# Performance work log

Measured on AMD Instinct MI355X. Metric: run time of the kernel, lower is better.

The kernel has to match this reference:

```python
import jax, jax.numpy as jnp
import numpy as np


def setup_inputs() -> dict:
    key = jax.random.key(0)
    ks = jax.random.split(key, 12)
    B, H, C, D, G, F = 2, 32, 256, 128, 2048, 128
    inp = {
        'k_c': jax.random.normal(ks[0], (B, H, C, D), jnp.float32),
        'v_c': jax.random.normal(ks[1], (B, H, C, D), jnp.float32),
        'fk_c': jax.random.uniform(ks[2], (B, H, C, F), jnp.float32),
        'score_c': jax.random.uniform(ks[3], (B, H, C), jnp.float32),
        'K_win': jax.random.normal(ks[4], (B, H, C, D), jnp.float32),
        'V_win': jax.random.normal(ks[5], (B, H, C, D), jnp.float32),
        'K_top': jax.random.normal(ks[6], (B, H, G, D), jnp.float32),
        'V_top': jax.random.normal(ks[7], (B, H, G, D), jnp.float32),
        'FK_top': jax.random.uniform(ks[8], (B, H, G, F), jnp.float32),
        'heap_val': jax.random.uniform(ks[9], (B, H, G), jnp.float32),
        'heap_idx': jax.random.randint(ks[10], (B, H, G), 0, 2048, jnp.int32),
        'tokens_seen': 4096,
    }
    return inp


def reference(k_c, v_c, fk_c, score_c, K_win, V_win, K_top, V_top, FK_top,
              heap_val, heap_idx, tokens_seen):
    # Steady-state LoLAState.train_chunk (heap and window already populated).
    B, H, C, D = k_c.shape
    G = heap_val.shape[-1]

    # Sliding window: drop oldest slot, append last token of chunk.
    K_win_new = jnp.concatenate([K_win[:, :, 1:], k_c[:, :, -1:]], axis=2)
    V_win_new = jnp.concatenate([V_win[:, :, 1:], v_c[:, :, -1:]], axis=2)

    # Global token indices for this chunk.
    chunk_idx = jnp.broadcast_to(
        (tokens_seen + jnp.arange(C, dtype=heap_idx.dtype))[None, None, :], (B, H, C))

    # Top-G eviction over [old heap | new chunk scores].
    cat_val = jnp.concatenate([heap_val, score_c], axis=-1)   # [B,H,G+C]
    cat_idx = jnp.concatenate([heap_idx, chunk_idx], axis=-1)  # [B,H,G+C]
    new_val, sel = jax.lax.top_k(cat_val, G)                   # sel in [0, G+C)
    new_idx = jnp.take_along_axis(cat_idx, sel, axis=-1)

    # Gather survivors from [old top | new chunk].
    prefix_K = jnp.concatenate([K_top, k_c], axis=2)    # [B,H,G+C,D]
    prefix_V = jnp.concatenate([V_top, v_c], axis=2)
    prefix_FK = jnp.concatenate([FK_top, fk_c], axis=2)
    sel4 = sel[..., None]
    K_top_new = jnp.take_along_axis(prefix_K, sel4, axis=2)
    V_top_new = jnp.take_along_axis(prefix_V, sel4, axis=2)
    FK_top_new = jnp.take_along_axis(prefix_FK, sel4, axis=2)

    # Low-rank sums (fp32, matching _recompute_sums).
    H_sum = jnp.einsum('bhgf,bhgd->bhfd', FK_top_new.astype(jnp.float32),
                       V_top_new.astype(jnp.float32))
    S_sum = FK_top_new.astype(jnp.float32).sum(axis=2)

    return (K_win_new, V_win_new, K_top_new, V_top_new, FK_top_new,
            new_val, new_idx, H_sum, S_sum)
```

## Files before the change

### kernel.cpp

```cpp
#include <hip/hip_runtime.h>
#include <stdint.h>

#define BB 2
#define HH 32
#define CC 256
#define DD 128
#define GG 2048
#define FF 128
#define NCAT (GG + CC)

__global__ __launch_bounds__(256) void rank_topk_kernel(
    const float* __restrict__ heap_val, const int* __restrict__ heap_idx,
    const float* __restrict__ score_c, const int* __restrict__ tokens_seen,
    float* __restrict__ out_val, float* __restrict__ out_idx,
    int* __restrict__ selws)
{
    __shared__ uint64_t keys[NCAT];

    const int blk = blockIdx.x;
    const int bh  = blk / 9;
    const int seg = blk - bh * 9;
    const int tid = threadIdx.x;

    const float* hv = heap_val + (size_t)bh * GG;
    const float* sc = score_c  + (size_t)bh * CC;

    for (int i = tid; i < NCAT; i += 256) {
        uint32_t fb = (i < GG) ? __float_as_uint(hv[i])
                               : __float_as_uint(sc[i - GG]);
        keys[i] = ((uint64_t)fb << 12) | (uint64_t)(4095 - i);
    }
    __syncthreads();

    const int cand = seg * 256 + tid;
    const uint64_t my = keys[cand];

    int rank = 0;
    const ulonglong2* k2 = (const ulonglong2*)keys;
#pragma unroll 4
    for (int j = 0; j < NCAT / 2; ++j) {
        ulonglong2 p = k2[j];
        rank += (p.x > my) + (p.y > my);
    }

    if (rank < GG) {
        const size_t o = (size_t)bh * GG + rank;
        out_val[o] = __uint_as_float((uint32_t)(my >> 12));
        int j = 4095 - (int)(my & 0xFFFull);
        int gidx = (j < GG) ? heap_idx[(size_t)bh * GG + j]
                            : (tokens_seen[0] + (j - GG));
        out_idx[o] = (float)gidx;
        selws[o] = j;
    }
}

__global__ __launch_bounds__(256) void fused_gather_hsum_kernel(
    const float4* __restrict__ K_top, const float4* __restrict__ V_top,
    const float4* __restrict__ FK_top,
    const float4* __restrict__ k_c, const float4* __restrict__ v_c,
    const float4* __restrict__ fk_c,
    const int* __restrict__ selws,
    float4* __restrict__ oK, float4* __restrict__ oV, float4* __restrict__ oFK,
    float* __restrict__ Hpart, float* __restrict__ Spart)
{
    __shared__ float fk_t[16][128];
    __shared__ float v_t[16][128];
    __shared__ float4 sredA[256];
    __shared__ float4 sredB[256];

    const int bh  = blockIdx.x >> 2;
    const int seg = blockIdx.x & 3;
    const int tid = threadIdx.x;
    const int r   = tid >> 4;
    const int q   = tid & 15;
    const int tf  = tid >> 4;
    const int td  = tid & 15;

    const long long topQ = (long long)bh * GG * 32;
    const long long chkQ = (long long)bh * CC * 32;
    const int row0 = seg * 512;
    const int selbase = bh * GG + row0;

    float acc[8][8];
#pragma unroll
    for (int a = 0; a < 8; ++a)
#pragma unroll
        for (int b2 = 0; b2 < 8; ++b2) acc[a][b2] = 0.f;
    float4 sA = make_float4(0.f, 0.f, 0.f, 0.f);
    float4 sB = make_float4(0.f, 0.f, 0.f, 0.f);

    int j = selws[selbase + r];
    const float4* bK = (j < GG) ? K_top  + topQ + (long long)j * 32
                                : k_c    + chkQ + (long long)(j - GG) * 32;
    const float4* bV = (j < GG) ? V_top  + topQ + (long long)j * 32
                                : v_c    + chkQ + (long long)(j - GG) * 32;
    const float4* bF = (j < GG) ? FK_top + topQ + (long long)j * 32
                                : fk_c   + chkQ + (long long)(j - GG) * 32;
    float4 pk0 = bK[q], pk1 = bK[q + 16];
    float4 pv0 = bV[q], pv1 = bV[q + 16];
    float4 pf0 = bF[q], pf1 = bF[q + 16];

    for (int tile = 0; tile < 32; ++tile) {
        const int gr = row0 + tile * 16;
        int jn = 0;
        if (tile < 31) jn = selws[selbase + tile * 16 + 16 + r];

        __syncthreads();
        *(float4*)&fk_t[r][q * 4]        = pf0;
        *(float4*)&fk_t[r][(q + 16) * 4] = pf1;
        *(float4*)&v_t[r][q * 4]         = pv0;
        *(float4*)&v_t[r][(q + 16) * 4]  = pv1;
        const long long ob = ((long long)bh * GG + gr + r) * 32;
        oFK[ob + q] = pf0;  oFK[ob + q + 16] = pf1;
        oV[ob + q]  = pv0;  oV[ob + q + 16]  = pv1;
        oK[ob + q]  = pk0;  oK[ob + q + 16]  = pk1;
        sA.x += pf0.x; sA.y += pf0.y; sA.z += pf0.z; sA.w += pf0.w;
        sB.x += pf1.x; sB.y += pf1.y; sB.z += pf1.z; sB.w += pf1.w;
        __syncthreads();

        if (tile < 31) {
            const float4* nK = (jn < GG) ? K_top  + topQ + (long long)jn * 32
                                         : k_c    + chkQ + (long long)(jn - GG) * 32;
            const float4* nV = (jn < GG) ? V_top  + topQ + (long long)jn * 32
                                         : v_c    + chkQ + (long long)(jn - GG) * 32;
            const float4* nF = (jn < GG) ? FK_top + topQ + (long long)jn * 32
                                         : fk_c   + chkQ + (long long)(jn - GG) * 32;
            pk0 = nK[q]; pk1 = nK[q + 16];
            pv0 = nV[q]; pv1 = nV[q + 16];
            pf0 = nF[q]; pf1 = nF[q + 16];
        }

#pragma unroll 4
        for (int g = 0; g < 16; ++g) {
            float4 fa0 = *(const float4*)&fk_t[g][tf * 8];
            float4 fa1 = *(const float4*)&fk_t[g][tf * 8 + 4];
            float4 vv0 = *(const float4*)&v_t[g][td * 8];
            float4 vv1 = *(const float4*)&v_t[g][td * 8 + 4];
            float fa[8] = {fa0.x, fa0.y, fa0.z, fa0.w, fa1.x, fa1.y, fa1.z, fa1.w};
            float vv[8] = {vv0.x, vv0.y, vv0.z, vv0.w, vv1.x, vv1.y, vv1.z, vv1.w};
#pragma unroll
            for (int a = 0; a < 8; ++a)
#pragma unroll
                for (int b2 = 0; b2 < 8; ++b2)
                    acc[a][b2] += fa[a] * vv[b2];
        }
    }

    float* Hb = Hpart + (long long)blockIdx.x * (FF * DD);
#pragma unroll
    for (int a = 0; a < 8; ++a) {
        *(float4*)&Hb[(long long)(tf * 8 + a) * DD + td * 8] =
            make_float4(acc[a][0], acc[a][1], acc[a][2], acc[a][3]);
        *(float4*)&Hb[(long long)(tf * 8 + a) * DD + td * 8 + 4] =
            make_float4(acc[a][4], acc[a][5], acc[a][6], acc[a][7]);
    }

    __syncthreads();
    sredA[tid] = sA; sredB[tid] = sB;
    __syncthreads();
    if (tid < 16) {
        float4 a = make_float4(0.f, 0.f, 0.f, 0.f);
        float4 b = make_float4(0.f, 0.f, 0.f, 0.f);
#pragma unroll
        for (int k = 0; k < 16; ++k) {
            float4 pa = sredA[k * 16 + tid];
            float4 pb = sredB[k * 16 + tid];
            a.x += pa.x; a.y += pa.y; a.z += pa.z; a.w += pa.w;
            b.x += pb.x; b.y += pb.y; b.z += pb.z; b.w += pb.w;
        }
        float* Sb = Spart + (long long)blockIdx.x * FF;
        *(float4*)&Sb[tid * 4]        = a;
        *(float4*)&Sb[(tid + 16) * 4] = b;
    }
}

__global__ __launch_bounds__(256) void finish_kernel(
    const float4* __restrict__ Hpart4, const float4* __restrict__ Spart4,
    const float4* __restrict__ K_win, const float4* __restrict__ V_win,
    const float4* __restrict__ k_c, const float4* __restrict__ v_c,
    float4* __restrict__ oKw, float4* __restrict__ oVw,
    float4* __restrict__ oH, float4* __restrict__ oS)
{
    const int b = blockIdx.x;
    const int tid = threadIdx.x;

    if (b < 4096) {
        const int QPA = BB * HH * CC * 32;
        int t = b * 256 + tid;
        int arr = t / QPA;
        int rem = t - arr * QPA;
        int row = rem >> 5;
        int q   = rem & 31;
        int bh  = row >> 8;
        int c   = row & 255;
        const float4* win = arr ? V_win : K_win;
        const float4* chk = arr ? v_c : k_c;
        float4 val = (c < CC - 1)
            ? win[((long long)bh * CC + c + 1) * 32 + q]
            : chk[((long long)bh * CC + (CC - 1)) * 32 + q];
        (arr ? oVw : oKw)[(long long)row * 32 + q] = val;
    } else if (b < 4096 + 1024) {
        int p  = (b - 4096) * 256 + tid;
        int bh = p >> 12;
        int off = p & 4095;
        float4 s = make_float4(0.f, 0.f, 0.f, 0.f);
#pragma unroll
        for (int s4 = 0; s4 < 4; ++s4) {
            float4 v = Hpart4[(((long long)bh * 4 + s4) << 12) + off];
            s.x += v.x; s.y += v.y; s.z += v.z; s.w += v.w;
        }
        oH[p] = s;
    } else {
        int p = (b - 5120) * 256 + tid;
        int bh = p >> 5;
        int off = p & 31;
        float4 s = make_float4(0.f, 0.f, 0.f, 0.f);
#pragma unroll
        for (int s4 = 0; s4 < 4; ++s4) {
            float4 v = Spart4[((long long)bh * 4 + s4) * 32 + off];
            s.x += v.x; s.y += v.y; s.z += v.z; s.w += v.w;
        }
        oS[p] = s;
    }
}

__global__ __launch_bounds__(256) void gather_topk_kernel(
    const float4* __restrict__ K_top, const float4* __restrict__ V_top,
    const float4* __restrict__ FK_top,
    const float4* __restrict__ k_c, const float4* __restrict__ v_c,
    const float4* __restrict__ fk_c,
    const int* __restrict__ selws,
    float4* __restrict__ oK, float4* __restrict__ oV, float4* __restrict__ oFK)
{
    const long long ROWQ = (long long)BB * HH * GG * 32;
    long long t = (long long)blockIdx.x * 256 + threadIdx.x;
    int arr = (int)(t / ROWQ);
    long long rem = t - (long long)arr * ROWQ;
    int row = (int)(rem >> 5);
    int q   = (int)(rem & 31);
    int bh  = row >> 11;
    int j   = selws[row];

    const float4* topsrc = (arr == 0) ? K_top : ((arr == 1) ? V_top : FK_top);
    const float4* chksrc = (arr == 0) ? k_c   : ((arr == 1) ? v_c   : fk_c);
    float4*       dst    = (arr == 0) ? oK    : ((arr == 1) ? oV    : oFK);

    float4 val;
    if (j < GG) val = topsrc[((long long)bh * GG + j) * 32 + q];
    else        val = chksrc[((long long)bh * CC + (j - GG)) * 32 + q];
    dst[(long long)row * 32 + q] = val;
}

__global__ __launch_bounds__(256) void window_kernel(
    const float4* __restrict__ K_win, const float4* __restrict__ V_win,
    const float4* __restrict__ k_c, const float4* __restrict__ v_c,
    float4* __restrict__ oKw, float4* __restrict__ oVw)
{
    const int QPA = BB * HH * CC * 32;
    int t = blockIdx.x * 256 + threadIdx.x;
    int arr = t / QPA;
    int rem = t - arr * QPA;
    int row = rem >> 5;
    int q   = rem & 31;
    int bh  = row >> 8;
    int c   = row & 255;

    const float4* win = arr ? V_win : K_win;
    const float4* chk = arr ? v_c : k_c;
    float4 val = (c < CC - 1)
        ? win[((long long)bh * CC + c + 1) * 32 + q]
        : chk[((long long)bh * CC + (CC - 1)) * 32 + q];
    (arr ? oVw : oKw)[(long long)row * 32 + q] = val;
}

__global__ __launch_bounds__(256) void hsum_kernel(
    const float4* __restrict__ FKq, const float4* __restrict__ Vq,
    float* __restrict__ H_out, float* __restrict__ S_out)
{
    __shared__ float fk_t[32][68];
    __shared__ float v_t[32][68];
    __shared__ float4 s4[256];

    const int bx  = blockIdx.x;
    const int bh  = bx >> 2;
    const int fq  = (bx >> 1) & 1;
    const int dq  = bx & 1;
    const int tid = threadIdx.x;
    const int g0 = tid >> 4;
    const int f4 = tid & 15;

    const float4* fkb = FKq + (long long)bh * GG * 32 + fq * 16 + f4;
    const float4* vb  = Vq  + (long long)bh * GG * 32 + dq * 16 + f4;

    float acc[4][4];
#pragma unroll
    for (int a = 0; a < 4; ++a)
#pragma unroll
        for (int b2 = 0; b2 < 4; ++b2) acc[a][b2] = 0.f;
    float4 s_acc = make_float4(0.f, 0.f, 0.f, 0.f);
    const int tf = tid >> 4, td = tid & 15;

    float4 pf_fk0 = fkb[(long long)(g0)      * 32];
    float4 pf_fk1 = fkb[(long long)(g0 + 16) * 32];
    float4 pf_v0  = vb [(long long)(g0)      * 32];
    float4 pf_v1  = vb [(long long)(g0 + 16) * 32];

    for (int c0 = 0; c0 < GG; c0 += 32) {
        __syncthreads();
        *(float4*)&fk_t[g0][f4 * 4]      = pf_fk0;
        *(float4*)&fk_t[g0 + 16][f4 * 4] = pf_fk1;
        *(float4*)&v_t[g0][f4 * 4]       = pf_v0;
        *(float4*)&v_t[g0 + 16][f4 * 4]  = pf_v1;
        s_acc.x += pf_fk0.x + pf_fk1.x;
        s_acc.y += pf_fk0.y + pf_fk1.y;
        s_acc.z += pf_fk0.z + pf_fk1.z;
        s_acc.w += pf_fk0.w + pf_fk1.w;
        __syncthreads();

        if (c0 + 32 < GG) {
            pf_fk0 = fkb[(long long)(c0 + 32 + g0)      * 32];
            pf_fk1 = fkb[(long long)(c0 + 32 + g0 + 16) * 32];
            pf_v0  = vb [(long long)(c0 + 32 + g0)      * 32];
            pf_v1  = vb [(long long)(c0 + 32 + g0 + 16) * 32];
        }

#pragma unroll 4
        for (int g = 0; g < 32; ++g) {
            float fa[4], vv[4];
#pragma unroll
            for (int a = 0; a < 4; ++a) fa[a] = fk_t[g][tf * 4 + a];
#pragma unroll
            for (int b2 = 0; b2 < 4; ++b2) vv[b2] = v_t[g][td * 4 + b2];
#pragma unroll
            for (int a = 0; a < 4; ++a)
#pragma unroll
                for (int b2 = 0; b2 < 4; ++b2)
                    acc[a][b2] += fa[a] * vv[b2];
        }
    }

    float* Hb = H_out + (long long)bh * FF * DD
              + (long long)(fq * 64 + tf * 4) * DD + dq * 64 + td * 4;
#pragma unroll
    for (int a = 0; a < 4; ++a)
        *(float4*)&Hb[(long long)a * DD] =
            make_float4(acc[a][0], acc[a][1], acc[a][2], acc[a][3]);

    s4[tid] = s_acc;
    __syncthreads();
    if (dq == 0 && tid < 16) {
        float4 s = make_float4(0.f, 0.f, 0.f, 0.f);
#pragma unroll
        for (int r = 0; r < 16; ++r) {
            float4 p = s4[r * 16 + tid];
            s.x += p.x; s.y += p.y; s.z += p.z; s.w += p.w;
        }
        *(float4*)&S_out[(long long)bh * FF + fq * 64 + tid * 4] = s;
    }
}

extern "C" void kernel_launch(void* const* d_in, const int* in_sizes, int n_in,
                              void* d_out, int out_size, void* d_ws, size_t ws_size,
                              hipStream_t stream) {
    const float* k_c      = (const float*)d_in[0];
    const float* v_c      = (const float*)d_in[1];
    const float* fk_c     = (const float*)d_in[2];
    const float* score_c  = (const float*)d_in[3];
    const float* K_win    = (const float*)d_in[4];
    const float* V_win    = (const float*)d_in[5];
    const float* K_top    = (const float*)d_in[6];
    const float* V_top    = (const float*)d_in[7];
    const float* FK_top   = (const float*)d_in[8];
    const float* heap_val = (const float*)d_in[9];
    const int*   heap_idx = (const int*)d_in[10];
    const int*   tokens   = (const int*)d_in[11];

    float* out = (float*)d_out;

    const size_t SZ_WIN = (size_t)BB * HH * CC * DD;
    const size_t SZ_TOP = (size_t)BB * HH * GG * DD;
    const size_t SZ_VAL = (size_t)BB * HH * GG;
    const size_t SZ_H   = (size_t)BB * HH * FF * DD;

    float* o_Kwin  = out;
    float* o_Vwin  = o_Kwin  + SZ_WIN;
    float* o_Ktop  = o_Vwin  + SZ_WIN;
    float* o_Vtop  = o_Ktop  + SZ_TOP;
    float* o_FKtop = o_Vtop  + SZ_TOP;
    float* o_val   = o_FKtop + SZ_TOP;
    float* o_idx   = o_val   + SZ_VAL;
    float* o_H     = o_idx   + SZ_VAL;
    float* o_S     = o_H     + SZ_H;

    const size_t selN   = (size_t)BB * HH * GG;
    const size_t hpartN = (size_t)256 * FF * DD;
    const size_t spartN = (size_t)256 * FF;
    const size_t need = selN * sizeof(int) + (hpartN + spartN) * sizeof(float);

    int*   selws = (int*)d_ws;
    float* Hpart = (float*)(selws + selN);
    float* Spart = Hpart + hpartN;

    rank_topk_kernel<<<BB * HH * 9, 256, 0, stream>>>(
        heap_val, heap_idx, score_c, tokens, o_val, o_idx, selws);

    if (ws_size >= need) {
        fused_gather_hsum_kernel<<<4 * BB * HH, 256, 0, stream>>>(
            (const float4*)K_top, (const float4*)V_top, (const float4*)FK_top,
            (const float4*)k_c, (const float4*)v_c, (const float4*)fk_c,
            selws, (float4*)o_Ktop, (float4*)o_Vtop, (float4*)o_FKtop,
            Hpart, Spart);

        finish_kernel<<<4096 + 1024 + 8, 256, 0, stream>>>(
            (const float4*)Hpart, (const float4*)Spart,
            (const float4*)K_win, (const float4*)V_win,
            (const float4*)k_c, (const float4*)v_c,
            (float4*)o_Kwin, (float4*)o_Vwin, (float4*)o_H, (float4*)o_S);
    } else {
        long long nthreads = 3LL * BB * HH * GG * 32;
        gather_topk_kernel<<<(int)(nthreads / 256), 256, 0, stream>>>(
            (const float4*)K_top, (const float4*)V_top, (const float4*)FK_top,
            (const float4*)k_c, (const float4*)v_c, (const float4*)fk_c,
            selws, (float4*)o_Ktop, (float4*)o_Vtop, (float4*)o_FKtop);
        int nthreads2 = 2 * BB * HH * CC * 32;
        window_kernel<<<nthreads2 / 256, 256, 0, stream>>>(
            (const float4*)K_win, (const float4*)V_win,
            (const float4*)k_c, (const float4*)v_c,
            (float4*)o_Kwin, (float4*)o_Vwin);
        hsum_kernel<<<4 * BB * HH, 256, 0, stream>>>(
            (const float4*)o_FKtop, (const float4*)o_Vtop, o_H, o_S);
    }
}
```

Measured before the change: 150.8 us.

## Split fused gather-hsum across more segments with 512-thread blocks

Raises the fused gather+H_sum kernel to 512 threads per block with 32-row tiles, and splits each (b,h) across up to 8 segments instead of 4, so 512 blocks run instead of 256. Each thread now holds an 8x4 accumulator instead of 8x6... 8x8, lowering register pressure. The aim is better occupancy and use of the GPU's compute units on a latency-bound gather. The cost is more partial H buffers to write and reduce in the finish kernel, plus a larger workspace requirement that falls back to 4 segments when the workspace is too small.

```diff
diff --git a/kernel.cpp b/kernel.cpp
--- a/kernel.cpp
+++ b/kernel.cpp
@@ -54,38 +54,40 @@
     }
 }
 
-__global__ __launch_bounds__(256) void fused_gather_hsum_kernel(
+__global__ __launch_bounds__(512) void fused_gather_hsum_kernel(
     const float4* __restrict__ K_top, const float4* __restrict__ V_top,
     const float4* __restrict__ FK_top,
     const float4* __restrict__ k_c, const float4* __restrict__ v_c,
     const float4* __restrict__ fk_c,
     const int* __restrict__ selws,
     float4* __restrict__ oK, float4* __restrict__ oV, float4* __restrict__ oFK,
-    float* __restrict__ Hpart, float* __restrict__ Spart)
-{
-    __shared__ float fk_t[16][128];
-    __shared__ float v_t[16][128];
-    __shared__ float4 sredA[256];
-    __shared__ float4 sredB[256];
-
-    const int bh  = blockIdx.x >> 2;
-    const int seg = blockIdx.x & 3;
+    float* __restrict__ Hpart, float* __restrict__ Spart, int nseg)
+{
+    __shared__ float fk_t[32][128];
+    __shared__ float v_t[32][128];
+    __shared__ float4 sredA[512];
+    __shared__ float4 sredB[512];
+
+    const int rows_pb = GG / nseg;
+    const int ntiles  = rows_pb / 32;
+    const int bh  = blockIdx.x / nseg;
+    const int seg = blockIdx.x - bh * nseg;
     const int tid = threadIdx.x;
     const int r   = tid >> 4;
     const int q   = tid & 15;
-    const int tf  = tid >> 4;
-    const int td  = tid & 15;
+    const int tf  = tid >> 5;
+    const int td  = tid & 31;
 
     const long long topQ = (long long)bh * GG * 32;
     const long long chkQ = (long long)bh * CC * 32;
-    const int row0 = seg * 512;
+    const int row0 = seg * rows_pb;
     const int selbase = bh * GG + row0;
 
-    float acc[8][8];
+    float acc[8][4];
 #pragma unroll
     for (int a = 0; a < 8; ++a)
 #pragma unroll
-        for (int b2 = 0; b2 < 8; ++b2) acc[a][b2] = 0.f;
+        for (int b2 = 0; b2 < 4; ++b2) acc[a][b2] = 0.f;
     float4 sA = make_float4(0.f, 0.f, 0.f, 0.f);
     float4 sB = make_float4(0.f, 0.f, 0.f, 0.f);
 
@@ -100,10 +102,10 @@
     float4 pv0 = bV[q], pv1 = bV[q + 16];
     float4 pf0 = bF[q], pf1 = bF[q + 16];
 
-    for (int tile = 0; tile < 32; ++tile) {
-        const int gr = row0 + tile * 16;
+    for (int tile = 0; tile < ntiles; ++tile) {
+        const int gr = row0 + tile * 32;
         int jn = 0;
-        if (tile < 31) jn = selws[selbase + tile * 16 + 16 + r];
+        if (tile < ntiles - 1) jn = selws[selbase + (tile + 1) * 32 + r];
 
         __syncthreads();
         *(float4*)&fk_t[r][q * 4]        = pf0;
@@ -118,7 +120,7 @@
         sB.x += pf1.x; sB.y += pf1.y; sB.z += pf1.z; sB.w += pf1.w;
         __syncthreads();
 
-        if (tile < 31) {
+        if (tile < ntiles - 1) {
             const float4* nK = (jn < GG) ? K_top  + topQ + (long long)jn * 32
                                          : k_c    + chkQ + (long long)(jn - GG) * 32;
             const float4* nV = (jn < GG) ? V_top  + topQ + (long long)jn * 32
@@ -131,29 +133,25 @@
         }
 
 #pragma unroll 4
-        for (int g = 0; g < 16; ++g) {
+        for (int g = 0; g < 32; ++g) {
             float4 fa0 = *(const float4*)&fk_t[g][tf * 8];
             float4 fa1 = *(const float4*)&fk_t[g][tf * 8 + 4];
-            float4 vv0 = *(const float4*)&v_t[g][td * 8];
-            float4 vv1 = *(const float4*)&v_t[g][td * 8 + 4];
+            float4 vvq = *(const float4*)&v_t[g][td * 4];
             float fa[8] = {fa0.x, fa0.y, fa0.z, fa0.w, fa1.x, fa1.y, fa1.z, fa1.w};
-            float vv[8] = {vv0.x, vv0.y, vv0.z, vv0.w, vv1.x, vv1.y, vv1.z, vv1.w};
+            float vv[4] = {vvq.x, vvq.y, vvq.z, vvq.w};
 #pragma unroll
             for (int a = 0; a < 8; ++a)
 #pragma unroll
-                for (int b2 = 0; b2 < 8; ++b2)
+                for (int b2 = 0; b2 < 4; ++b2)
                     acc[a][b2] += fa[a] * vv[b2];
         }
     }
 
     float* Hb = Hpart + (long long)blockIdx.x * (FF * DD);
 #pragma unroll
-    for (int a = 0; a < 8; ++a) {
-        *(float4*)&Hb[(long long)(tf * 8 + a) * DD + td * 8] =
+    for (int a = 0; a < 8; ++a)
+        *(float4*)&Hb[(long long)(tf * 8 + a) * DD + td * 4] =
             make_float4(acc[a][0], acc[a][1], acc[a][2], acc[a][3]);
-        *(float4*)&Hb[(long long)(tf * 8 + a) * DD + td * 8 + 4] =
-            make_float4(acc[a][4], acc[a][5], acc[a][6], acc[a][7]);
-    }
 
     __syncthreads();
     sredA[tid] = sA; sredB[tid] = sB;
@@ -162,7 +160,7 @@
         float4 a = make_float4(0.f, 0.f, 0.f, 0.f);
         float4 b = make_float4(0.f, 0.f, 0.f, 0.f);
 #pragma unroll
-        for (int k = 0; k < 16; ++k) {
+        for (int k = 0; k < 32; ++k) {
             float4 pa = sredA[k * 16 + tid];
             float4 pb = sredB[k * 16 + tid];
             a.x += pa.x; a.y += pa.y; a.z += pa.z; a.w += pa.w;
@@ -179,7 +177,7 @@
     const float4* __restrict__ K_win, const float4* __restrict__ V_win,
     const float4* __restrict__ k_c, const float4* __restrict__ v_c,
     float4* __restrict__ oKw, float4* __restrict__ oVw,
-    float4* __restrict__ oH, float4* __restrict__ oS)
+    float4* __restrict__ oH, float4* __restrict__ oS, int nseg)
 {
     const int b = blockIdx.x;
     const int tid = threadIdx.x;
@@ -204,9 +202,8 @@
         int bh = p >> 12;
         int off = p & 4095;
         float4 s = make_float4(0.f, 0.f, 0.f, 0.f);
-#pragma unroll
-        for (int s4 = 0; s4 < 4; ++s4) {
-            float4 v = Hpart4[(((long long)bh * 4 + s4) << 12) + off];
+        for (int s4 = 0; s4 < nseg; ++s4) {
+            float4 v = Hpart4[(((long long)bh * nseg + s4) << 12) + off];
             s.x += v.x; s.y += v.y; s.z += v.z; s.w += v.w;
         }
         oH[p] = s;
@@ -215,9 +212,8 @@
         int bh = p >> 5;
         int off = p & 31;
         float4 s = make_float4(0.f, 0.f, 0.f, 0.f);
-#pragma unroll
-        for (int s4 = 0; s4 < 4; ++s4) {
-            float4 v = Spart4[((long long)bh * 4 + s4) * 32 + off];
+        for (int s4 = 0; s4 < nseg; ++s4) {
+            float4 v = Spart4[((long long)bh * nseg + s4) * 32 + off];
             s.x += v.x; s.y += v.y; s.z += v.z; s.w += v.w;
         }
         oS[p] = s;
@@ -392,30 +388,34 @@
     float* o_H     = o_idx   + SZ_VAL;
     float* o_S     = o_H     + SZ_H;
 
-    const size_t selN   = (size_t)BB * HH * GG;
-    const size_t hpartN = (size_t)256 * FF * DD;
-    const size_t spartN = (size_t)256 * FF;
-    const size_t need = selN * sizeof(int) + (hpartN + spartN) * sizeof(float);
+    const size_t selN = (size_t)BB * HH * GG;
+
+    int nseg = 8;
+    size_t need8 = selN * sizeof(int)
+                 + (size_t)(BB * HH * 8) * (FF * DD + FF) * sizeof(float);
+    size_t need4 = selN * sizeof(int)
+                 + (size_t)(BB * HH * 4) * (FF * DD + FF) * sizeof(float);
+    if (ws_size < need8) nseg = 4;
 
     int*   selws = (int*)d_ws;
     float* Hpart = (float*)(selws + selN);
-    float* Spart = Hpart + hpartN;
+    float* Spart = Hpart + (size_t)(BB * HH * nseg) * FF * DD;
 
     rank_topk_kernel<<<BB * HH * 9, 256, 0, stream>>>(
         heap_val, heap_idx, score_c, tokens, o_val, o_idx, selws);
 
-    if (ws_size >= need) {
-        fused_gather_hsum_kernel<<<4 * BB * HH, 256, 0, stream>>>(
+    if (ws_size >= need4) {
+        fused_gather_hsum_kernel<<<BB * HH * nseg, 512, 0, stream>>>(
             (const float4*)K_top, (const float4*)V_top, (const float4*)FK_top,
             (const float4*)k_c, (const float4*)v_c, (const float4*)fk_c,
             selws, (float4*)o_Ktop, (float4*)o_Vtop, (float4*)o_FKtop,
-            Hpart, Spart);
+            Hpart, Spart, nseg);
 
         finish_kernel<<<4096 + 1024 + 8, 256, 0, stream>>>(
             (const float4*)Hpart, (const float4*)Spart,
             (const float4*)K_win, (const float4*)V_win,
             (const float4*)k_c, (const float4*)v_c,
-            (float4*)o_Kwin, (float4*)o_Vwin, (float4*)o_H, (float4*)o_S);
+            (float4*)o_Kwin, (float4*)o_Vwin, (float4*)o_H, (float4*)o_S, nseg);
     } else {
         long long nthreads = 3LL * BB * HH * GG * 32;
         gather_topk_kernel<<<(int)(nthreads / 256), 256, 0, stream>>>(
```

Measured after the change: 158.8 us. +5.3%, slower.
